# Optimization experiments

Hardware: AMD Instinct MI355X
Metric: run time of the kernel (lower is better)

The kernel has to match this reference:

```python
import jax, jax.numpy as jnp
import numpy as np


def setup_inputs() -> dict:
    key = jax.random.key(0)
    k1, k2, k3, k4 = jax.random.split(key, 4)
    batch, T, state_dim, action_dim = 64, 1024, 512, 128
    x0 = jax.random.normal(k1, (batch, state_dim), dtype=jnp.float32)
    us = jax.random.normal(k2, (batch, T, action_dim), dtype=jnp.float32)
    # Scale A so the 1024-step linear recurrence stays bounded (spectral radius < 1)
    A = jax.random.normal(k3, (state_dim, state_dim), dtype=jnp.float32) * (0.9 / np.sqrt(state_dim))
    B = jax.random.normal(k4, (action_dim, state_dim), dtype=jnp.float32) * (1.0 / np.sqrt(action_dim))
    return {"x0": x0, "us": us, "A": A, "B": B}


def reference(x0, us, A, B):
    """Linear SSM rollout: x_{t+1} = x_t @ A + u_t @ B, returns xs [batch, T, state_dim]."""
    us_t = jnp.swapaxes(us, 0, 1)  # [T, batch, action_dim]

    def step(x, u):
        x_next = x @ A + u @ B  # [batch, state_dim]
        return x_next, x_next

    _, xs = jax.lax.scan(step, x0, us_t)  # xs: [T, batch, state_dim]
    return jnp.swapaxes(xs, 0, 1)  # [batch, T, state_dim]
```

## Files before the change

### kernel.cpp

```cpp
#include <hip/hip_runtime.h>


typedef __attribute__((ext_vector_type(8))) short bf16x8;
typedef __attribute__((ext_vector_type(8))) unsigned short ushort8;
typedef __attribute__((ext_vector_type(4))) float f32x4;
typedef unsigned short ushort_t;

#define MFMA16(a, b, c) __builtin_amdgcn_mfma_f32_16x16x32_bf16(a, b, c, 0, 0, 0)

#define OFF_AT  0UL
#define OFF_AU  8912896UL
#define OFF_BT  15204352UL
#define OFF_BU  15335424UL
#define OFF_X0B 15466496UL
#define OFF_YPK 15532032UL
#define OFF_Z   23920640UL
#define OFF_ZS  49086464UL
#define OFF_E2  58523648UL

__host__ __device__ __forceinline__ int slot_of(int p) {
    if (p == 0) return 16;
    if (p <= 8) return p - 1;
    return 7 + (p >> 3);
}

__device__ __forceinline__ unsigned short f2bf(float f) {
    union { float f; unsigned u; } v; v.f = f;
    unsigned r = v.u + 0x7FFFu + ((v.u >> 16) & 1u);
    return (unsigned short)(r >> 16);
}

__device__ __forceinline__ float bf2f(ushort_t h) {
    union { unsigned u; float f; } v; v.u = ((unsigned)h) << 16; return v.f;
}

__device__ __forceinline__ int sel4(int4 v, int p) {
    return p == 0 ? v.x : p == 1 ? v.y : p == 2 ? v.z : v.w;
}

typedef __attribute__((address_space(3))) unsigned int as3_u32;
typedef __attribute__((address_space(1))) const unsigned int as1_u32;
__device__ __forceinline__ void gll16(const void* g, void* l) {
    __builtin_amdgcn_global_load_lds((as1_u32*)g, (as3_u32*)l, 16, 0, 0);
}

__global__ __launch_bounds__(256) void prep_kernel(const float* __restrict__ x0,
                                                   const float* __restrict__ us,
                                                   const float* __restrict__ A,
                                                   const float* __restrict__ B,
                                                   char* __restrict__ ws) {
    ushort_t* At1 = (ushort_t*)(ws + OFF_AT);
    ushort_t* Au1 = (ushort_t*)(ws + OFF_AU);
    ushort_t* Bt  = (ushort_t*)(ws + OFF_BT);
    ushort_t* Bu  = (ushort_t*)(ws + OFF_BU);
    ushort_t* X0b = (ushort_t*)(ws + OFF_X0B);
    ushort_t* Z   = (ushort_t*)(ws + OFF_Z);
    long idx = (long)blockIdx.x * 256 + threadIdx.x;
    if (idx < 262144) {
        int k = (int)(idx >> 9), n = (int)(idx & 511);
        ushort_t v = f2bf(A[idx]);
        Au1[idx] = v;
        At1[(long)n * 512 + k] = v;
    } else if (idx < 327680) {
        long i2 = idx - 262144;
        int kp = (int)(i2 >> 9), n = (int)(i2 & 511);
        ushort_t v = f2bf(B[i2]);
        Bt[(long)n * 128 + kp] = v;
        Bu[i2] = v;
    } else if (idx < 331776) {
        long gi = idx - 327680;
        long e0 = gi * 8;
        float4 v0 = *(const float4*)(x0 + e0);
        float4 v1 = *(const float4*)(x0 + e0 + 4);
        ushort8 h = { f2bf(v0.x), f2bf(v0.y), f2bf(v0.z), f2bf(v0.w),
                      f2bf(v1.x), f2bf(v1.y), f2bf(v1.z), f2bf(v1.w) };
        *(ushort8*)(X0b + e0) = h;
    } else if (idx < 1380352) {
        long gi = idx - 331776;
        int row = (int)(gi >> 7), g8 = (int)(gi & 127);
        int c = row >> 6, b = row & 63;
        const float* src = us + (long)b * 131072 + c * 1024 + g8 * 8;
        float4 v0 = *(const float4*)src;
        float4 v1 = *(const float4*)(src + 4);
        ushort8 h = { f2bf(v0.x), f2bf(v0.y), f2bf(v0.z), f2bf(v0.w),
                      f2bf(v1.x), f2bf(v1.y), f2bf(v1.z), f2bf(v1.w) };
        *(ushort8*)(Z + (long)row * 1536 + 512 + g8 * 8) = h;
    } else {
        long gi2 = idx - 1380352;
        if (gi2 < 262144) {
            int n = (int)(gi2 >> 9), k2 = (int)(gi2 & 511);
            At1[(long)16 * 262144 + gi2] = (n == k2) ? (ushort_t)0x3F80 : (ushort_t)0;
        }
    }
}

__global__ __launch_bounds__(256) void pow_stage(char* __restrict__ ws,
                                                 int4 dd, int4 mm, int4 ii, int dual) {
    __shared__ ushort_t ldsX[64 * 512];
    ushort_t* At = (ushort_t*)(ws + OFF_AT);
    ushort_t* Au = (ushort_t*)(ws + OFF_AU);

    int bx = blockIdx.x;
    int nb = bx & 3, mb = (bx >> 2) & 7;
    int prod, pair;
    if (dual) { prod = (bx >> 5) & 1; pair = bx >> 6; }
    else      { prod = 0;             pair = bx >> 5; }
    int d = sel4(dd, pair), m_ = sel4(mm, pair), i_ = sel4(ii, pair);

    const ushort_t *Xp, *Yp; ushort_t* outp;
    if (prod == 0) { Xp = At + (long)slot_of(m_) * 262144; Yp = Au + (long)slot_of(i_) * 262144; outp = At + (long)slot_of(d) * 262144; }
    else           { Xp = Au + (long)slot_of(i_) * 262144; Yp = At + (long)slot_of(m_) * 262144; outp = Au + (long)slot_of(d) * 262144; }

    int tid = threadIdx.x, w = tid >> 6, lane = tid & 63, q = lane >> 4, r = lane & 15;

    for (int i2 = tid; i2 < 64 * 64; i2 += 256) {
        int row = i2 >> 6, c8 = i2 & 63;
        ushort8 v = *(const ushort8*)(Xp + (long)(mb * 64 + row) * 512 + c8 * 8);
        *(ushort8*)&ldsX[row * 512 + ((c8 ^ (row & 7)) << 3)] = v;
    }
    __syncthreads();

    f32x4 acc[4][2];
    for (int a1 = 0; a1 < 4; a1++) for (int b1 = 0; b1 < 2; b1++) acc[a1][b1] = (f32x4){0.f, 0.f, 0.f, 0.f};

    int n0 = nb * 128 + w * 32;
    for (int kt = 0; kt < 16; kt++) {
        bf16x8 b0 = *(const bf16x8*)(Yp + (long)(n0 + r) * 512 + kt * 32 + q * 8);
        bf16x8 b1 = *(const bf16x8*)(Yp + (long)(n0 + 16 + r) * 512 + kt * 32 + q * 8);
        int g2 = kt * 4 + q;
#pragma unroll
        for (int mi = 0; mi < 4; mi++) {
            int row = mi * 16 + r;
            bf16x8 a = *(bf16x8*)&ldsX[row * 512 + ((g2 ^ (row & 7)) << 3)];
            acc[mi][0] = MFMA16(a, b0, acc[mi][0]);
            acc[mi][1] = MFMA16(a, b1, acc[mi][1]);
        }
    }
    for (int mi = 0; mi < 4; mi++) for (int nj = 0; nj < 2; nj++) {
        int m = mb * 64 + mi * 16 + q * 4, n = n0 + nj * 16 + r;
        for (int v = 0; v < 4; v++) outp[(long)(m + v) * 512 + n] = f2bf(acc[mi][nj][v]);
    }
}

__global__ __launch_bounds__(256) void wk_kernel(char* __restrict__ ws) {
    __shared__ ushort_t ldsX[64 * 512];
    ushort_t* At = (ushort_t*)(ws + OFF_AT);
    ushort_t* Bu = (ushort_t*)(ws + OFF_BU);
    ushort_t* Bt = (ushort_t*)(ws + OFF_BT);
    ushort_t* Ypk = (ushort_t*)(ws + OFF_YPK);

    int bx = blockIdx.x;
    int k8 = bx >> 3, mb = bx & 7;
    int tid = threadIdx.x, w = tid >> 6, lane = tid & 63, q = lane >> 4, r = lane & 15;

    if (k8 == 7) {
        for (int i2 = tid; i2 < 64 * 32; i2 += 256) {
            int row = i2 >> 5, c4 = i2 & 31;
            ushort4 v = *(const ushort4*)(Bt + (long)(mb * 64 + row) * 128 + c4 * 4);
            for (int k = 0; k < 8; k++)
                *(ushort4*)(Ypk + (long)k * 524288 + (long)(mb * 64 + row) * 1024 + k * 128 + c4 * 4) = v;
        }
        return;
    }

    int p = 7 - k8;
    const ushort_t* Xp = At + (long)slot_of(p) * 262144;
    for (int i2 = tid; i2 < 64 * 64; i2 += 256) {
        int row = i2 >> 6, c8 = i2 & 63;
        ushort8 v = *(const ushort8*)(Xp + (long)(mb * 64 + row) * 512 + c8 * 8);
        *(ushort8*)&ldsX[row * 512 + ((c8 ^ (row & 7)) << 3)] = v;
    }
    __syncthreads();

    f32x4 acc[4][2];
    for (int a1 = 0; a1 < 4; a1++) for (int b1 = 0; b1 < 2; b1++) acc[a1][b1] = (f32x4){0.f, 0.f, 0.f, 0.f};

    int n0 = w * 32;
    for (int kt = 0; kt < 16; kt++) {
        bf16x8 b0 = *(const bf16x8*)(Bu + (long)(n0 + r) * 512 + kt * 32 + q * 8);
        bf16x8 b1 = *(const bf16x8*)(Bu + (long)(n0 + 16 + r) * 512 + kt * 32 + q * 8);
        int g2 = kt * 4 + q;
#pragma unroll
        for (int mi = 0; mi < 4; mi++) {
            int row = mi * 16 + r;
            bf16x8 a = *(bf16x8*)&ldsX[row * 512 + ((g2 ^ (row & 7)) << 3)];
            acc[mi][0] = MFMA16(a, b0, acc[mi][0]);
            acc[mi][1] = MFMA16(a, b1, acc[mi][1]);
        }
    }
    for (int mi = 0; mi < 4; mi++) for (int nj = 0; nj < 2; nj++) {
        int m = mb * 64 + mi * 16 + q * 4, n = n0 + nj * 16 + r;
        for (int v = 0; v < 4; v++) {
            ushort_t h = f2bf(acc[mi][nj][v]);
            for (int k = p; k < 8; k++)
                Ypk[(long)k * 524288 + (long)(m + v) * 1024 + (k - p) * 128 + n] = h;
        }
    }
}

__global__ __launch_bounds__(256, 4) void e1g(char* __restrict__ ws) {
    __shared__ ushort_t Alds[64 * 64];
    __shared__ ushort_t Blds[128 * 64];
    const ushort_t* Z   = (const ushort_t*)(ws + OFF_Z);
    const ushort_t* Yw  = (const ushort_t*)(ws + OFF_YPK) + 7 * 524288;
    ushort_t* Zs = (ushort_t*)(ws + OFF_ZS);

    int bx = blockIdx.x;
    int c = bx >> 2, nt = bx & 3;
    int tid = threadIdx.x, w = tid >> 6, lane = tid & 63, q = lane >> 4, r = lane & 15;
    int wr = w >> 1, wc = w & 1;
    int l8 = lane >> 3, srcg = (lane & 7) ^ l8;

    f32x4 acc[2][4];
#pragma unroll
    for (int a1 = 0; a1 < 2; a1++)
#pragma unroll
        for (int b1 = 0; b1 < 4; b1++) acc[a1][b1] = (f32x4){0.f, 0.f, 0.f, 0.f};

    for (int s = 0; s < 16; s++) {
        int k0 = s * 64;
#pragma unroll
        for (int i = 0; i < 2; i++) {
            int row = i * 32 + w * 8 + l8;
            gll16(Z + (long)(c * 64 + row) * 1536 + 512 + k0 + srcg * 8,
                  &Alds[i * 2048 + w * 512]);
        }
#pragma unroll
        for (int i = 0; i < 4; i++) {
            int row = i * 32 + w * 8 + l8;
            gll16(Yw + (long)(nt * 128 + row) * 1024 + k0 + srcg * 8,
                  &Blds[i * 2048 + w * 512]);
        }
        __syncthreads();
#pragma unroll
        for (int kt = 0; kt < 2; kt++) {
            int g2 = kt * 4 + q;
            bf16x8 a[2], b[4];
#pragma unroll
            for (int mi = 0; mi < 2; mi++) {
                int row = wr * 32 + mi * 16 + r;
                a[mi] = *(bf16x8*)&Alds[row * 64 + ((g2 ^ (row & 7)) << 3)];
            }
#pragma unroll
            for (int nj = 0; nj < 4; nj++) {
                int row = wc * 64 + nj * 16 + r;
                b[nj] = *(bf16x8*)&Blds[row * 64 + ((g2 ^ (row & 7)) << 3)];
            }
#pragma unroll
            for (int mi = 0; mi < 2; mi++)
#pragma unroll
                for (int nj = 0; nj < 4; nj++)
                    acc[mi][nj] = MFMA16(a[mi], b[nj], acc[mi][nj]);
        }
        __syncthreads();
    }

    int g = c >> 3, cc = c & 7;
#pragma unroll
    for (int mi = 0; mi < 2; mi++)
#pragma unroll
        for (int nj = 0; nj < 4; nj++) {
            int brow = wr * 32 + mi * 16 + q * 4;
            int n = nt * 128 + wc * 64 + nj * 16 + r;
#pragma unroll
            for (int v = 0; v < 4; v++)
                Zs[(long)(g * 64 + brow + v) * 4608 + (1 + cc) * 512 + n] = f2bf(acc[mi][nj][v]);
        }
}

__global__ __launch_bounds__(256, 4) void e2g(char* __restrict__ ws) {
    __shared__ ushort_t Alds[64 * 64];
    __shared__ ushort_t Blds[64 * 64];
    const ushort_t* Zs = (const ushort_t*)(ws + OFF_ZS);
    const ushort_t* At = (const ushort_t*)(ws + OFF_AT);
    ushort_t* E2b = (ushort_t*)(ws + OFF_E2);

    int bx = blockIdx.x;
    int g = bx >> 3, ntb = bx & 7;
    int tid = threadIdx.x, w = tid >> 6, lane = tid & 63, q = lane >> 4, r = lane & 15;
    int wr = w >> 1, wc = w & 1;
    int l8 = lane >> 3, srcg = (lane & 7) ^ l8;

    f32x4 acc[2][2];
#pragma unroll
    for (int a1 = 0; a1 < 2; a1++)
#pragma unroll
        for (int b1 = 0; b1 < 2; b1++) acc[a1][b1] = (f32x4){0.f, 0.f, 0.f, 0.f};

    for (int s = 0; s < 8; s++) {
        const ushort_t* Yb = At + (long)slot_of(8 * (7 - s)) * 262144;
        for (int ks = 0; ks < 8; ks++) {
            int k0 = ks * 64;
#pragma unroll
            for (int i = 0; i < 2; i++) {
                int row = i * 32 + w * 8 + l8;
                gll16(Zs + (long)(g * 64 + row) * 4608 + (1 + s) * 512 + k0 + srcg * 8,
                      &Alds[i * 2048 + w * 512]);
                gll16(Yb + (long)(ntb * 64 + row) * 512 + k0 + srcg * 8,
                      &Blds[i * 2048 + w * 512]);
            }
            __syncthreads();
#pragma unroll
            for (int kt = 0; kt < 2; kt++) {
                int g2 = kt * 4 + q;
                bf16x8 a[2], b[2];
#pragma unroll
                for (int mi = 0; mi < 2; mi++) {
                    int row = wr * 32 + mi * 16 + r;
                    a[mi] = *(bf16x8*)&Alds[row * 64 + ((g2 ^ (row & 7)) << 3)];
                }
#pragma unroll
                for (int nj = 0; nj < 2; nj++) {
                    int row = wc * 32 + nj * 16 + r;
                    b[nj] = *(bf16x8*)&Blds[row * 64 + ((g2 ^ (row & 7)) << 3)];
                }
#pragma unroll
                for (int mi = 0; mi < 2; mi++)
#pragma unroll
                    for (int nj = 0; nj < 2; nj++)
                        acc[mi][nj] = MFMA16(a[mi], b[nj], acc[mi][nj]);
            }
            __syncthreads();
        }
    }

#pragma unroll
    for (int mi = 0; mi < 2; mi++)
#pragma unroll
        for (int nj = 0; nj < 2; nj++) {
            int brow = wr * 32 + mi * 16 + q * 4;
            int n = ntb * 64 + wc * 32 + nj * 16 + r;
#pragma unroll
            for (int v = 0; v < 4; v++)
                E2b[(long)g * 32768 + (long)(brow + v) * 512 + n] = f2bf(acc[mi][nj][v]);
        }
}

__global__ __launch_bounds__(256) void s2k(char* __restrict__ ws) {
    __shared__ ushort_t ldsX[64 * 512];
    ushort_t* At  = (ushort_t*)(ws + OFF_AT);
    ushort_t* E2b = (ushort_t*)(ws + OFF_E2);
    ushort_t* X0b = (ushort_t*)(ws + OFF_X0B);
    ushort_t* Zs  = (ushort_t*)(ws + OFF_ZS);

    int bx = blockIdx.x;
    int g = bx >> 2, nb = bx & 3;
    int tid = threadIdx.x, w = tid >> 6, lane = tid & 63, q = lane >> 4, r = lane & 15;

    int nterms = (g == 0) ? 1 : 2;

    f32x4 acc[4][2];
    for (int a1 = 0; a1 < 4; a1++) for (int b1 = 0; b1 < 2; b1++) acc[a1][b1] = (f32x4){0.f, 0.f, 0.f, 0.f};

    for (int t = 0; t < nterms; t++) {
        const ushort_t* X; const ushort_t* Y = nullptr;
        if (g == 0) { X = X0b; }
        else if (t == 0) { X = E2b + (long)(g - 1) * 32768; }
        else if (g == 1) { X = X0b; Y = At + (long)slot_of(64) * 262144; }
        else { X = E2b + (long)(g - 2) * 32768; Y = At + (long)slot_of(64) * 262144; }

        if (Y == nullptr) {
            int n0 = nb * 128 + w * 32;
            for (int mi = 0; mi < 4; mi++) for (int nj = 0; nj < 2; nj++) {
                int m = mi * 16 + q * 4, n = n0 + nj * 16 + r;
                for (int v = 0; v < 4; v++) acc[mi][nj][v] += bf2f(X[(long)(m + v) * 512 + n]);
            }
        } else {
            __syncthreads();
            for (int i2 = tid; i2 < 64 * 64; i2 += 256) {
                int row = i2 >> 6, c8 = i2 & 63;
                ushort8 v = *(const ushort8*)(X + (long)row * 512 + c8 * 8);
                *(ushort8*)&ldsX[row * 512 + ((c8 ^ (row & 7)) << 3)] = v;
            }
            __syncthreads();
            int n0 = nb * 128 + w * 32;
            for (int kt = 0; kt < 16; kt++) {
                bf16x8 b0 = *(const bf16x8*)(Y + (long)(n0 + r) * 512 + kt * 32 + q * 8);
                bf16x8 b1 = *(const bf16x8*)(Y + (long)(n0 + 16 + r) * 512 + kt * 32 + q * 8);
                int g2 = kt * 4 + q;
#pragma unroll
                for (int mi = 0; mi < 4; mi++) {
                    int row = mi * 16 + r;
                    bf16x8 a = *(bf16x8*)&ldsX[row * 512 + ((g2 ^ (row & 7)) << 3)];
                    acc[mi][0] = MFMA16(a, b0, acc[mi][0]);
                    acc[mi][1] = MFMA16(a, b1, acc[mi][1]);
                }
            }
        }
    }

    int n0 = nb * 128 + w * 32;
    for (int mi = 0; mi < 4; mi++) for (int nj = 0; nj < 2; nj++) {
        int m = mi * 16 + q * 4, n = n0 + nj * 16 + r;
        for (int v = 0; v < 4; v++)
            Zs[(long)(g * 64 + m + v) * 4608 + n] = f2bf(acc[mi][nj][v]);
    }
}

__global__ __launch_bounds__(256, 4) void s1g(char* __restrict__ ws) {
    __shared__ ushort_t Alds[64 * 64];
    __shared__ ushort_t Blds[128 * 64];
    const ushort_t* Zs = (const ushort_t*)(ws + OFF_ZS);
    const ushort_t* At = (const ushort_t*)(ws + OFF_AT);
    ushort_t* Z = (ushort_t*)(ws + OFF_Z);

    int bx = blockIdx.x;
    int j = bx & 7, nt = (bx >> 3) & 3, g = bx >> 5;
    int tid = threadIdx.x, w = tid >> 6, lane = tid & 63, q = lane >> 4, r = lane & 15;
    int wr = w >> 1, wc = w & 1;
    int l8 = lane >> 3, srcg = (lane & 7) ^ l8;

    f32x4 acc[2][4];
#pragma unroll
    for (int a1 = 0; a1 < 2; a1++)
#pragma unroll
        for (int b1 = 0; b1 < 4; b1++) acc[a1][b1] = (f32x4){0.f, 0.f, 0.f, 0.f};

    for (int s = 0; s <= j; s++) {
        int p = (s == 0) ? 8 * j : 8 * (j - s);
        const ushort_t* Yb = At + (long)slot_of(p) * 262144;
        for (int ks = 0; ks < 8; ks++) {
            int k0 = ks * 64;
#pragma unroll
            for (int i = 0; i < 2; i++) {
                int row = i * 32 + w * 8 + l8;
                gll16(Zs + (long)(g * 64 + row) * 4608 + s * 512 + k0 + srcg * 8,
                      &Alds[i * 2048 + w * 512]);
            }
#pragma unroll
            for (int i = 0; i < 4; i++) {
                int row = i * 32 + w * 8 + l8;
                gll16(Yb + (long)(nt * 128 + row) * 512 + k0 + srcg * 8,
                      &Blds[i * 2048 + w * 512]);
            }
            __syncthreads();
#pragma unroll
            for (int kt = 0; kt < 2; kt++) {
                int g2 = kt * 4 + q;
                bf16x8 a[2], b[4];
#pragma unroll
                for (int mi = 0; mi < 2; mi++) {
                    int row = wr * 32 + mi * 16 + r;
                    a[mi] = *(bf16x8*)&Alds[row * 64 + ((g2 ^ (row & 7)) << 3)];
                }
#pragma unroll
                for (int nj = 0; nj < 4; nj++) {
                    int row = wc * 64 + nj * 16 + r;
                    b[nj] = *(bf16x8*)&Blds[row * 64 + ((g2 ^ (row & 7)) << 3)];
                }
#pragma unroll
                for (int mi = 0; mi < 2; mi++)
#pragma unroll
                    for (int nj = 0; nj < 4; nj++)
                        acc[mi][nj] = MFMA16(a[mi], b[nj], acc[mi][nj]);
            }
            __syncthreads();
        }
    }

#pragma unroll
    for (int mi = 0; mi < 2; mi++)
#pragma unroll
        for (int nj = 0; nj < 4; nj++) {
            int brow = wr * 32 + mi * 16 + q * 4;
            int n = nt * 128 + wc * 64 + nj * 16 + r;
#pragma unroll
            for (int v = 0; v < 4; v++)
                Z[(long)(g * 512 + j * 64 + brow + v) * 1536 + n] = f2bf(acc[mi][nj][v]);
        }
}

__global__ __launch_bounds__(256, 4) void outg(float* __restrict__ dout,
                                               char* __restrict__ ws) {
    __shared__ ushort_t Alds[128 * 64];
    __shared__ ushort_t Blds[128 * 64];
    const ushort_t* Z   = (const ushort_t*)(ws + OFF_Z);
    const ushort_t* At  = (const ushort_t*)(ws + OFF_AT);
    const ushort_t* Ypk = (const ushort_t*)(ws + OFF_YPK);

    int bx = blockIdx.x;
    int mt = bx & 63;
    int k  = (bx >> 6) & 7;
    int nt = bx >> 9;
    int tid = threadIdx.x, w = tid >> 6, lane = tid & 63, q = lane >> 4, r = lane & 15;
    int wr = w >> 1, wc = w & 1;

    int Ks = 8 + 2 * (k + 1);
    const ushort_t* Ya = At + (long)slot_of(k + 1) * 262144;
    const ushort_t* Yu = Ypk + (long)k * 524288;

    int l8 = lane >> 3;
    int srcg = (lane & 7) ^ l8;

    f32x4 acc[4][4];
#pragma unroll
    for (int a1 = 0; a1 < 4; a1++)
#pragma unroll
        for (int b1 = 0; b1 < 4; b1++) acc[a1][b1] = (f32x4){0.f, 0.f, 0.f, 0.f};

    for (int s = 0; s < Ks; s++) {
        int k0 = s * 64;
#pragma unroll
        for (int i = 0; i < 4; i++) {
            int row = i * 32 + w * 8 + l8;
            gll16(Z + (long)(mt * 128 + row) * 1536 + k0 + srcg * 8,
                  &Alds[i * 2048 + w * 512]);
        }
        if (k0 < 512) {
#pragma unroll
            for (int i = 0; i < 4; i++) {
                int row = i * 32 + w * 8 + l8;
                gll16(Ya + (long)(nt * 128 + row) * 512 + k0 + srcg * 8,
                      &Blds[i * 2048 + w * 512]);
            }
        } else {
#pragma unroll
            for (int i = 0; i < 4; i++) {
                int row = i * 32 + w * 8 + l8;
                gll16(Yu + (long)(nt * 128 + row) * 1024 + (k0 - 512) + srcg * 8,
                      &Blds[i * 2048 + w * 512]);
            }
        }
        __syncthreads();
#pragma unroll
        for (int kt = 0; kt < 2; kt++) {
            int g2 = kt * 4 + q;
            bf16x8 a[4], b[4];
#pragma unroll
            for (int mi = 0; mi < 4; mi++) {
                int row = wr * 64 + mi * 16 + r;
                a[mi] = *(bf16x8*)&Alds[row * 64 + ((g2 ^ (row & 7)) << 3)];
            }
#pragma unroll
            for (int nj = 0; nj < 4; nj++) {
                int row = wc * 64 + nj * 16 + r;
                b[nj] = *(bf16x8*)&Blds[row * 64 + ((g2 ^ (row & 7)) << 3)];
            }
#pragma unroll
            for (int mi = 0; mi < 4; mi++)
#pragma unroll
                for (int nj = 0; nj < 4; nj++)
                    acc[mi][nj] = MFMA16(a[mi], b[nj], acc[mi][nj]);
        }
        __syncthreads();
    }

#pragma unroll
    for (int mi = 0; mi < 4; mi++) {
        int m = mt * 128 + wr * 64 + mi * 16 + q * 4;
#pragma unroll
        for (int nj = 0; nj < 4; nj++) {
            int n = nt * 128 + wc * 64 + nj * 16 + r;
#pragma unroll
            for (int v = 0; v < 4; v++) {
                int mm = m + v;
                dout[(long)(mm & 63) * 524288 + (long)(((mm >> 6) << 3) + k) * 512 + n] = acc[mi][nj][v];
            }
        }
    }
}

extern "C" void kernel_launch(void* const* d_in, const int* in_sizes, int n_in,
                              void* d_out, int out_size, void* d_ws, size_t ws_size,
                              hipStream_t stream) {
    const float* x0 = (const float*)d_in[0];
    const float* us = (const float*)d_in[1];
    const float* A  = (const float*)d_in[2];
    const float* B  = (const float*)d_in[3];
    float* dout = (float*)d_out;
    char* ws = (char*)d_ws;

    prep_kernel<<<6416, 256, 0, stream>>>(x0, us, A, B, ws);

    const int stn[6]     = {1, 2, 4, 1, 2, 4};
    const int stdual[6]  = {1, 1, 1, 1, 1, 0};
    const int std_[6][4] = {{2,0,0,0},{3,4,0,0},{5,6,7,8},{16,0,0,0},{24,32,0,0},{40,48,56,64}};
    const int stm[6][4]  = {{1,0,0,0},{2,2,0,0},{4,4,4,4},{8,0,0,0},{16,16,0,0},{32,32,32,32}};
    const int sti[6][4]  = {{1,0,0,0},{1,2,0,0},{1,2,3,4},{8,0,0,0},{8,16,0,0},{8,16,24,32}};
    for (int s = 0; s < 6; s++) {
        int4 dd = {std_[s][0], std_[s][1], std_[s][2], std_[s][3]};
        int4 mm = {stm[s][0], stm[s][1], stm[s][2], stm[s][3]};
        int4 ii = {sti[s][0], sti[s][1], sti[s][2], sti[s][3]};
        int blocks = stn[s] * (stdual[s] ? 64 : 32);
        pow_stage<<<blocks, 256, 0, stream>>>(ws, dd, mm, ii, stdual[s]);
    }

    wk_kernel<<<64, 256, 0, stream>>>(ws);
    e1g<<<512, 256, 0, stream>>>(ws);
    e2g<<<128, 256, 0, stream>>>(ws);
    s2k<<<64, 256, 0, stream>>>(ws);
    s1g<<<512, 256, 0, stream>>>(ws);
    outg<<<2048, 256, 0, stream>>>(dout, ws);
}
```

Baseline: 290.8 us.

## Restructure chunked scan stages with double-buffered LDS and direct global B loads

```diff
diff --git a/kernel.cpp b/kernel.cpp
--- a/kernel.cpp
+++ b/kernel.cpp
@@ -12,11 +12,10 @@
 #define OFF_AU  8912896UL
 #define OFF_BT  15204352UL
 #define OFF_BU  15335424UL
-#define OFF_X0B 15466496UL
-#define OFF_YPK 15532032UL
-#define OFF_Z   23920640UL
-#define OFF_ZS  49086464UL
-#define OFF_E2  58523648UL
+#define OFF_WT  15466496UL
+#define OFF_Z   16515072UL
+#define OFF_E1S 41680896UL
+#define OFF_E2S 50069504UL
 
 __host__ __device__ __forceinline__ int slot_of(int p) {
     if (p == 0) return 16;
@@ -28,10 +27,6 @@
     union { float f; unsigned u; } v; v.f = f;
     unsigned r = v.u + 0x7FFFu + ((v.u >> 16) & 1u);
     return (unsigned short)(r >> 16);
-}
-
-__device__ __forceinline__ float bf2f(ushort_t h) {
-    union { unsigned u; float f; } v; v.u = ((unsigned)h) << 16; return v.f;
 }
 
 __device__ __forceinline__ int sel4(int4 v, int p) {
@@ -53,7 +48,7 @@
     ushort_t* Au1 = (ushort_t*)(ws + OFF_AU);
     ushort_t* Bt  = (ushort_t*)(ws + OFF_BT);
     ushort_t* Bu  = (ushort_t*)(ws + OFF_BU);
-    ushort_t* X0b = (ushort_t*)(ws + OFF_X0B);
+    ushort_t* X0b = (ushort_t*)(ws + OFF_E2S);
     ushort_t* Z   = (ushort_t*)(ws + OFF_Z);
     long idx = (long)blockIdx.x * 256 + threadIdx.x;
     if (idx < 262144) {
@@ -147,7 +142,7 @@
     ushort_t* At = (ushort_t*)(ws + OFF_AT);
     ushort_t* Bu = (ushort_t*)(ws + OFF_BU);
     ushort_t* Bt = (ushort_t*)(ws + OFF_BT);
-    ushort_t* Ypk = (ushort_t*)(ws + OFF_YPK);
+    ushort_t* Wt = (ushort_t*)(ws + OFF_WT);
 
     int bx = blockIdx.x;
     int k8 = bx >> 3, mb = bx & 7;
@@ -157,8 +152,7 @@
         for (int i2 = tid; i2 < 64 * 32; i2 += 256) {
             int row = i2 >> 5, c4 = i2 & 31;
             ushort4 v = *(const ushort4*)(Bt + (long)(mb * 64 + row) * 128 + c4 * 4);
-            for (int k = 0; k < 8; k++)
-                *(ushort4*)(Ypk + (long)k * 524288 + (long)(mb * 64 + row) * 1024 + k * 128 + c4 * 4) = v;
+            *(ushort4*)(Wt + (long)(mb * 64 + row) * 128 + c4 * 4) = v;
         }
         return;
     }
@@ -188,22 +182,18 @@
             acc[mi][1] = MFMA16(a, b1, acc[mi][1]);
         }
     }
+    ushort_t* Wp = Wt + (long)p * 65536;
     for (int mi = 0; mi < 4; mi++) for (int nj = 0; nj < 2; nj++) {
         int m = mb * 64 + mi * 16 + q * 4, n = n0 + nj * 16 + r;
-        for (int v = 0; v < 4; v++) {
-            ushort_t h = f2bf(acc[mi][nj][v]);
-            for (int k = p; k < 8; k++)
-                Ypk[(long)k * 524288 + (long)(m + v) * 1024 + (k - p) * 128 + n] = h;
-        }
-    }
-}
-
-__global__ __launch_bounds__(256, 4) void e1g(char* __restrict__ ws) {
-    __shared__ ushort_t Alds[64 * 64];
-    __shared__ ushort_t Blds[128 * 64];
-    const ushort_t* Z   = (const ushort_t*)(ws + OFF_Z);
-    const ushort_t* Yw  = (const ushort_t*)(ws + OFF_YPK) + 7 * 524288;
-    ushort_t* Zs = (ushort_t*)(ws + OFF_ZS);
+        for (int v = 0; v < 4; v++) Wp[(long)(m + v) * 128 + n] = f2bf(acc[mi][nj][v]);
+    }
+}
+
+__global__ __launch_bounds__(256) void e1g(char* __restrict__ ws) {
+    __shared__ ushort_t Alds[2][64 * 64];
+    const ushort_t* Z  = (const ushort_t*)(ws + OFF_Z);
+    const ushort_t* Wt = (const ushort_t*)(ws + OFF_WT);
+    ushort_t* E1s = (ushort_t*)(ws + OFF_E1S);
 
     int bx = blockIdx.x;
     int c = bx >> 2, nt = bx & 3;
@@ -211,27 +201,33 @@
     int wr = w >> 1, wc = w & 1;
     int l8 = lane >> 3, srcg = (lane & 7) ^ l8;
 
+    const ushort_t* Xb = Z + (long)c * 64 * 1536 + 512;
+
     f32x4 acc[2][4];
 #pragma unroll
     for (int a1 = 0; a1 < 2; a1++)
 #pragma unroll
         for (int b1 = 0; b1 < 4; b1++) acc[a1][b1] = (f32x4){0.f, 0.f, 0.f, 0.f};
 
+#pragma unroll
+    for (int i = 0; i < 2; i++) {
+        int row = i * 32 + w * 8 + l8;
+        gll16(Xb + (long)row * 1536 + srcg * 8, &Alds[0][i * 2048 + w * 512]);
+    }
+    __syncthreads();
+
+    int cur = 0;
     for (int s = 0; s < 16; s++) {
-        int k0 = s * 64;
-#pragma unroll
-        for (int i = 0; i < 2; i++) {
-            int row = i * 32 + w * 8 + l8;
-            gll16(Z + (long)(c * 64 + row) * 1536 + 512 + k0 + srcg * 8,
-                  &Alds[i * 2048 + w * 512]);
-        }
-#pragma unroll
-        for (int i = 0; i < 4; i++) {
-            int row = i * 32 + w * 8 + l8;
-            gll16(Yw + (long)(nt * 128 + row) * 1024 + k0 + srcg * 8,
-                  &Blds[i * 2048 + w * 512]);
-        }
-        __syncthreads();
+        if (s + 1 < 16) {
+            int kn = (s + 1) * 64;
+#pragma unroll
+            for (int i = 0; i < 2; i++) {
+                int row = i * 32 + w * 8 + l8;
+                gll16(Xb + (long)row * 1536 + kn + srcg * 8, &Alds[cur ^ 1][i * 2048 + w * 512]);
+            }
+        }
+        const ushort_t* Yb = Wt + (long)(7 - (s >> 1)) * 65536;
+        int sub = (s & 1) * 64;
 #pragma unroll
         for (int kt = 0; kt < 2; kt++) {
             int g2 = kt * 4 + q;
@@ -239,12 +235,12 @@
 #pragma unroll
             for (int mi = 0; mi < 2; mi++) {
                 int row = wr * 32 + mi * 16 + r;
-                a[mi] = *(bf16x8*)&Alds[row * 64 + ((g2 ^ (row & 7)) << 3)];
+                a[mi] = *(bf16x8*)&Alds[cur][row * 64 + ((g2 ^ (row & 7)) << 3)];
             }
 #pragma unroll
             for (int nj = 0; nj < 4; nj++) {
-                int row = wc * 64 + nj * 16 + r;
-                b[nj] = *(bf16x8*)&Blds[row * 64 + ((g2 ^ (row & 7)) << 3)];
+                int n = nt * 128 + wc * 64 + nj * 16 + r;
+                b[nj] = *(const bf16x8*)(Yb + (long)n * 128 + sub + kt * 32 + q * 8);
             }
 #pragma unroll
             for (int mi = 0; mi < 2; mi++)
@@ -253,230 +249,194 @@
                     acc[mi][nj] = MFMA16(a[mi], b[nj], acc[mi][nj]);
         }
         __syncthreads();
-    }
-
-    int g = c >> 3, cc = c & 7;
+        cur ^= 1;
+    }
+
 #pragma unroll
     for (int mi = 0; mi < 2; mi++)
 #pragma unroll
         for (int nj = 0; nj < 4; nj++) {
-            int brow = wr * 32 + mi * 16 + q * 4;
+            int m = wr * 32 + mi * 16 + q * 4;
             int n = nt * 128 + wc * 64 + nj * 16 + r;
 #pragma unroll
             for (int v = 0; v < 4; v++)
-                Zs[(long)(g * 64 + brow + v) * 4608 + (1 + cc) * 512 + n] = f2bf(acc[mi][nj][v]);
-        }
-}
-
-__global__ __launch_bounds__(256, 4) void e2g(char* __restrict__ ws) {
-    __shared__ ushort_t Alds[64 * 64];
-    __shared__ ushort_t Blds[64 * 64];
-    const ushort_t* Zs = (const ushort_t*)(ws + OFF_ZS);
-    const ushort_t* At = (const ushort_t*)(ws + OFF_AT);
-    ushort_t* E2b = (ushort_t*)(ws + OFF_E2);
+                E1s[(long)c * 32768 + (long)(m + v) * 512 + n] = f2bf(acc[mi][nj][v]);
+        }
+}
+
+__global__ __launch_bounds__(256) void e2g(char* __restrict__ ws) {
+    __shared__ ushort_t Alds[2][64 * 64];
+    const ushort_t* At  = (const ushort_t*)(ws + OFF_AT);
+    const ushort_t* E1s = (const ushort_t*)(ws + OFF_E1S);
+    ushort_t* E2s = (ushort_t*)(ws + OFF_E2S);
 
     int bx = blockIdx.x;
-    int g = bx >> 3, ntb = bx & 7;
+    int g = bx >> 2, nt = bx & 3;
     int tid = threadIdx.x, w = tid >> 6, lane = tid & 63, q = lane >> 4, r = lane & 15;
     int wr = w >> 1, wc = w & 1;
     int l8 = lane >> 3, srcg = (lane & 7) ^ l8;
 
-    f32x4 acc[2][2];
+    f32x4 acc[2][4];
 #pragma unroll
     for (int a1 = 0; a1 < 2; a1++)
 #pragma unroll
-        for (int b1 = 0; b1 < 2; b1++) acc[a1][b1] = (f32x4){0.f, 0.f, 0.f, 0.f};
-
-    for (int s = 0; s < 8; s++) {
-        const ushort_t* Yb = At + (long)slot_of(8 * (7 - s)) * 262144;
-        for (int ks = 0; ks < 8; ks++) {
-            int k0 = ks * 64;
+        for (int b1 = 0; b1 < 4; b1++) acc[a1][b1] = (f32x4){0.f, 0.f, 0.f, 0.f};
+
+#pragma unroll
+    for (int i = 0; i < 2; i++) {
+        int row = i * 32 + w * 8 + l8;
+        gll16(E1s + (long)(8 * g) * 32768 + (long)row * 512 + srcg * 8,
+              &Alds[0][i * 2048 + w * 512]);
+    }
+    __syncthreads();
+
+    int cur = 0;
+    for (int s = 0; s < 64; s++) {
+        if (s + 1 < 64) {
+            int t2 = (s + 1) >> 3, kn = ((s + 1) & 7) * 64;
+            const ushort_t* Xp = E1s + (long)(8 * g + t2) * 32768;
 #pragma unroll
             for (int i = 0; i < 2; i++) {
                 int row = i * 32 + w * 8 + l8;
-                gll16(Zs + (long)(g * 64 + row) * 4608 + (1 + s) * 512 + k0 + srcg * 8,
-                      &Alds[i * 2048 + w * 512]);
-                gll16(Yb + (long)(ntb * 64 + row) * 512 + k0 + srcg * 8,
-                      &Blds[i * 2048 + w * 512]);
-            }
-            __syncthreads();
-#pragma unroll
-            for (int kt = 0; kt < 2; kt++) {
-                int g2 = kt * 4 + q;
-                bf16x8 a[2], b[2];
-#pragma unroll
-                for (int mi = 0; mi < 2; mi++) {
-                    int row = wr * 32 + mi * 16 + r;
-                    a[mi] = *(bf16x8*)&Alds[row * 64 + ((g2 ^ (row & 7)) << 3)];
-                }
-#pragma unroll
-                for (int nj = 0; nj < 2; nj++) {
-                    int row = wc * 32 + nj * 16 + r;
-                    b[nj] = *(bf16x8*)&Blds[row * 64 + ((g2 ^ (row & 7)) << 3)];
-                }
-#pragma unroll
-                for (int mi = 0; mi < 2; mi++)
-#pragma unroll
-                    for (int nj = 0; nj < 2; nj++)
-                        acc[mi][nj] = MFMA16(a[mi], b[nj], acc[mi][nj]);
-            }
-            __syncthreads();
-        }
+                gll16(Xp + (long)row * 512 + kn + srcg * 8, &Alds[cur ^ 1][i * 2048 + w * 512]);
+            }
+        }
+        int t = s >> 3, k0 = (s & 7) * 64;
+        const ushort_t* Yb = At + (long)slot_of(8 * (7 - t)) * 262144;
+#pragma unroll
+        for (int kt = 0; kt < 2; kt++) {
+            int g2 = kt * 4 + q;
+            bf16x8 a[2], b[4];
+#pragma unroll
+            for (int mi = 0; mi < 2; mi++) {
+                int row = wr * 32 + mi * 16 + r;
+                a[mi] = *(bf16x8*)&Alds[cur][row * 64 + ((g2 ^ (row & 7)) << 3)];
+            }
+#pragma unroll
+            for (int nj = 0; nj < 4; nj++) {
+                int n = nt * 128 + wc * 64 + nj * 16 + r;
+                b[nj] = *(const bf16x8*)(Yb + (long)n * 512 + k0 + kt * 32 + q * 8);
+            }
+#pragma unroll
+            for (int mi = 0; mi < 2; mi++)
+#pragma unroll
+                for (int nj = 0; nj < 4; nj++)
+                    acc[mi][nj] = MFMA16(a[mi], b[nj], acc[mi][nj]);
+        }
+        __syncthreads();
+        cur ^= 1;
     }
 
 #pragma unroll
     for (int mi = 0; mi < 2; mi++)
 #pragma unroll
-        for (int nj = 0; nj < 2; nj++) {
-            int brow = wr * 32 + mi * 16 + q * 4;
-            int n = ntb * 64 + wc * 32 + nj * 16 + r;
+        for (int nj = 0; nj < 4; nj++) {
+            int m = wr * 32 + mi * 16 + q * 4;
+            int n = nt * 128 + wc * 64 + nj * 16 + r;
 #pragma unroll
             for (int v = 0; v < 4; v++)
-                E2b[(long)g * 32768 + (long)(brow + v) * 512 + n] = f2bf(acc[mi][nj][v]);
-        }
-}
-
-__global__ __launch_bounds__(256) void s2k(char* __restrict__ ws) {
-    __shared__ ushort_t ldsX[64 * 512];
-    ushort_t* At  = (ushort_t*)(ws + OFF_AT);
-    ushort_t* E2b = (ushort_t*)(ws + OFF_E2);
-    ushort_t* X0b = (ushort_t*)(ws + OFF_X0B);
-    ushort_t* Zs  = (ushort_t*)(ws + OFF_ZS);
+                E2s[(long)(1 + g) * 32768 + (long)(m + v) * 512 + n] = f2bf(acc[mi][nj][v]);
+        }
+}
+
+__global__ __launch_bounds__(256) void s1x(char* __restrict__ ws) {
+    __shared__ ushort_t Alds[2][64 * 64];
+    const ushort_t* At  = (const ushort_t*)(ws + OFF_AT);
+    const ushort_t* E1s = (const ushort_t*)(ws + OFF_E1S);
+    const ushort_t* E2s = (const ushort_t*)(ws + OFF_E2S);
+    ushort_t* Z = (ushort_t*)(ws + OFF_Z);
 
     int bx = blockIdx.x;
-    int g = bx >> 2, nb = bx & 3;
-    int tid = threadIdx.x, w = tid >> 6, lane = tid & 63, q = lane >> 4, r = lane & 15;
-
-    int nterms = (g == 0) ? 1 : 2;
-
-    f32x4 acc[4][2];
-    for (int a1 = 0; a1 < 4; a1++) for (int b1 = 0; b1 < 2; b1++) acc[a1][b1] = (f32x4){0.f, 0.f, 0.f, 0.f};
-
-    for (int t = 0; t < nterms; t++) {
-        const ushort_t* X; const ushort_t* Y = nullptr;
-        if (g == 0) { X = X0b; }
-        else if (t == 0) { X = E2b + (long)(g - 1) * 32768; }
-        else if (g == 1) { X = X0b; Y = At + (long)slot_of(64) * 262144; }
-        else { X = E2b + (long)(g - 2) * 32768; Y = At + (long)slot_of(64) * 262144; }
-
-        if (Y == nullptr) {
-            int n0 = nb * 128 + w * 32;
-            for (int mi = 0; mi < 4; mi++) for (int nj = 0; nj < 2; nj++) {
-                int m = mi * 16 + q * 4, n = n0 + nj * 16 + r;
-                for (int v = 0; v < 4; v++) acc[mi][nj][v] += bf2f(X[(long)(m + v) * 512 + n]);
-            }
-        } else {
-            __syncthreads();
-            for (int i2 = tid; i2 < 64 * 64; i2 += 256) {
-                int row = i2 >> 6, c8 = i2 & 63;
-                ushort8 v = *(const ushort8*)(X + (long)row * 512 + c8 * 8);
-                *(ushort8*)&ldsX[row * 512 + ((c8 ^ (row & 7)) << 3)] = v;
-            }
-            __syncthreads();
-            int n0 = nb * 128 + w * 32;
-            for (int kt = 0; kt < 16; kt++) {
-                bf16x8 b0 = *(const bf16x8*)(Y + (long)(n0 + r) * 512 + kt * 32 + q * 8);
-                bf16x8 b1 = *(const bf16x8*)(Y + (long)(n0 + 16 + r) * 512 + kt * 32 + q * 8);
-                int g2 = kt * 4 + q;
-#pragma unroll
-                for (int mi = 0; mi < 4; mi++) {
-                    int row = mi * 16 + r;
-                    bf16x8 a = *(bf16x8*)&ldsX[row * 512 + ((g2 ^ (row & 7)) << 3)];
-                    acc[mi][0] = MFMA16(a, b0, acc[mi][0]);
-                    acc[mi][1] = MFMA16(a, b1, acc[mi][1]);
-                }
-            }
-        }
-    }
-
-    int n0 = nb * 128 + w * 32;
-    for (int mi = 0; mi < 4; mi++) for (int nj = 0; nj < 2; nj++) {
-        int m = mi * 16 + q * 4, n = n0 + nj * 16 + r;
-        for (int v = 0; v < 4; v++)
-            Zs[(long)(g * 64 + m + v) * 4608 + n] = f2bf(acc[mi][nj][v]);
-    }
-}
-
-__global__ __launch_bounds__(256, 4) void s1g(char* __restrict__ ws) {
-    __shared__ ushort_t Alds[64 * 64];
-    __shared__ ushort_t Blds[128 * 64];
-    const ushort_t* Zs = (const ushort_t*)(ws + OFF_ZS);
-    const ushort_t* At = (const ushort_t*)(ws + OFF_AT);
-    ushort_t* Z = (ushort_t*)(ws + OFF_Z);
-
-    int bx = blockIdx.x;
-    int j = bx & 7, nt = (bx >> 3) & 3, g = bx >> 5;
+    int c = bx >> 2, nt = bx & 3;
+    int g = c >> 3, j = c & 7;
+    int extra = (j == 0 && g >= 1) ? 1 : 0;
+    int nterms = 1 + extra + j;
+    int S = nterms * 8;
     int tid = threadIdx.x, w = tid >> 6, lane = tid & 63, q = lane >> 4, r = lane & 15;
     int wr = w >> 1, wc = w & 1;
     int l8 = lane >> 3, srcg = (lane & 7) ^ l8;
 
+    auto xptr = [&](int t) -> const ushort_t* {
+        if (t == 0) return E2s + (long)g * 32768;
+        if (extra && t == 1) return E2s + (long)(g - 1) * 32768;
+        return E1s + (long)(8 * g + t - 1 - extra) * 32768;
+    };
+    auto yptr = [&](int t) -> const ushort_t* {
+        int p = (t == 0) ? 8 * j : ((extra && t == 1) ? 64 : 8 * (j - t + extra));
+        return At + (long)slot_of(p) * 262144;
+    };
+
     f32x4 acc[2][4];
 #pragma unroll
     for (int a1 = 0; a1 < 2; a1++)
 #pragma unroll
         for (int b1 = 0; b1 < 4; b1++) acc[a1][b1] = (f32x4){0.f, 0.f, 0.f, 0.f};
 
-    for (int s = 0; s <= j; s++) {
-        int p = (s == 0) ? 8 * j : 8 * (j - s);
-        const ushort_t* Yb = At + (long)slot_of(p) * 262144;
-        for (int ks = 0; ks < 8; ks++) {
-            int k0 = ks * 64;
+    {
+        const ushort_t* Xp = xptr(0);
+#pragma unroll
+        for (int i = 0; i < 2; i++) {
+            int row = i * 32 + w * 8 + l8;
+            gll16(Xp + (long)row * 512 + srcg * 8, &Alds[0][i * 2048 + w * 512]);
+        }
+    }
+    __syncthreads();
+
+    int cur = 0;
+    for (int s = 0; s < S; s++) {
+        if (s + 1 < S) {
+            const ushort_t* Xp = xptr((s + 1) >> 3);
+            int kn = ((s + 1) & 7) * 64;
 #pragma unroll
             for (int i = 0; i < 2; i++) {
                 int row = i * 32 + w * 8 + l8;
-                gll16(Zs + (long)(g * 64 + row) * 4608 + s * 512 + k0 + srcg * 8,
-                      &Alds[i * 2048 + w * 512]);
-            }
-#pragma unroll
-            for (int i = 0; i < 4; i++) {
-                int row = i * 32 + w * 8 + l8;
-                gll16(Yb + (long)(nt * 128 + row) * 512 + k0 + srcg * 8,
-                      &Blds[i * 2048 + w * 512]);
-            }
-            __syncthreads();
-#pragma unroll
-            for (int kt = 0; kt < 2; kt++) {
-                int g2 = kt * 4 + q;
-                bf16x8 a[2], b[4];
-#pragma unroll
-                for (int mi = 0; mi < 2; mi++) {
-                    int row = wr * 32 + mi * 16 + r;
-                    a[mi] = *(bf16x8*)&Alds[row * 64 + ((g2 ^ (row & 7)) << 3)];
-                }
-#pragma unroll
-                for (int nj = 0; nj < 4; nj++) {
-                    int row = wc * 64 + nj * 16 + r;
-                    b[nj] = *(bf16x8*)&Blds[row * 64 + ((g2 ^ (row & 7)) << 3)];
-                }
-#pragma unroll
-                for (int mi = 0; mi < 2; mi++)
-#pragma unroll
-                    for (int nj = 0; nj < 4; nj++)
-                        acc[mi][nj] = MFMA16(a[mi], b[nj], acc[mi][nj]);
-            }
-            __syncthreads();
-        }
+                gll16(Xp + (long)row * 512 + kn + srcg * 8, &Alds[cur ^ 1][i * 2048 + w * 512]);
+            }
+        }
+        int k0 = (s & 7) * 64;
+        const ushort_t* Yb = yptr(s >> 3);
+#pragma unroll
+        for (int kt = 0; kt < 2; kt++) {
+            int g2 = kt * 4 + q;
+            bf16x8 a[2], b[4];
+#pragma unroll
+            for (int mi = 0; mi < 2; mi++) {
+                int row = wr * 32 + mi * 16 + r;
+                a[mi] = *(bf16x8*)&Alds[cur][row * 64 + ((g2 ^ (row & 7)) << 3)];
+            }
+#pragma unroll
+            for (int nj = 0; nj < 4; nj++) {
+                int n = nt * 128 + wc * 64 + nj * 16 + r;
+                b[nj] = *(const bf16x8*)(Yb + (long)n * 512 + k0 + kt * 32 + q * 8);
+            }
+#pragma unroll
+            for (int mi = 0; mi < 2; mi++)
+#pragma unroll
+                for (int nj = 0; nj < 4; nj++)
+                    acc[mi][nj] = MFMA16(a[mi], b[nj], acc[mi][nj]);
+        }
+        __syncthreads();
+        cur ^= 1;
     }
 
 #pragma unroll
     for (int mi = 0; mi < 2; mi++)
 #pragma unroll
         for (int nj = 0; nj < 4; nj++) {
-            int brow = wr * 32 + mi * 16 + q * 4;
+            int m = wr * 32 + mi * 16 + q * 4;
             int n = nt * 128 + wc * 64 + nj * 16 + r;
 #pragma unroll
             for (int v = 0; v < 4; v++)
-                Z[(long)(g * 512 + j * 64 + brow + v) * 1536 + n] = f2bf(acc[mi][nj][v]);
-        }
-}
-
-__global__ __launch_bounds__(256, 4) void outg(float* __restrict__ dout,
-                                               char* __restrict__ ws) {
-    __shared__ ushort_t Alds[128 * 64];
-    __shared__ ushort_t Blds[128 * 64];
-    const ushort_t* Z   = (const ushort_t*)(ws + OFF_Z);
-    const ushort_t* At  = (const ushort_t*)(ws + OFF_AT);
-    const ushort_t* Ypk = (const ushort_t*)(ws + OFF_YPK);
+                Z[(long)(c * 64 + m + v) * 1536 + n] = f2bf(acc[mi][nj][v]);
+        }
+}
+
+__global__ __launch_bounds__(256) void outg(float* __restrict__ dout,
+                                            char* __restrict__ ws) {
+    __shared__ ushort_t Alds[2][128 * 64];
+    const ushort_t* Z  = (const ushort_t*)(ws + OFF_Z);
+    const ushort_t* At = (const ushort_t*)(ws + OFF_AT);
+    const ushort_t* Wt = (const ushort_t*)(ws + OFF_WT);
 
     int bx = blockIdx.x;
     int mt = bx & 63;
@@ -484,13 +444,11 @@
     int nt = bx >> 9;
     int tid = threadIdx.x, w = tid >> 6, lane = tid & 63, q = lane >> 4, r = lane & 15;
     int wr = w >> 1, wc = w & 1;
-
+    int l8 = lane >> 3, srcg = (lane & 7) ^ l8;
+
+    const ushort_t* Xb = Z + (long)mt * 128 * 1536;
+    const ushort_t* Ya = At + (long)slot_of(k + 1) * 262144;
     int Ks = 8 + 2 * (k + 1);
-    const ushort_t* Ya = At + (long)slot_of(k + 1) * 262144;
-    const ushort_t* Yu = Ypk + (long)k * 524288;
-
-    int l8 = lane >> 3;
-    int srcg = (lane & 7) ^ l8;
 
     f32x4 acc[4][4];
 #pragma unroll
@@ -498,30 +456,27 @@
 #pragma unroll
         for (int b1 = 0; b1 < 4; b1++) acc[a1][b1] = (f32x4){0.f, 0.f, 0.f, 0.f};
 
+#pragma unroll
+    for (int i = 0; i < 4; i++) {
+        int row = i * 32 + w * 8 + l8;
+        gll16(Xb + (long)row * 1536 + srcg * 8, &Alds[0][i * 2048 + w * 512]);
+    }
+    __syncthreads();
+
+    int cur = 0;
     for (int s = 0; s < Ks; s++) {
-        int k0 = s * 64;
-#pragma unroll
-        for (int i = 0; i < 4; i++) {
-            int row = i * 32 + w * 8 + l8;
-            gll16(Z + (long)(mt * 128 + row) * 1536 + k0 + srcg * 8,
-                  &Alds[i * 2048 + w * 512]);
-        }
-        if (k0 < 512) {
+        if (s + 1 < Ks) {
+            int kn = (s + 1) * 64;
 #pragma unroll
             for (int i = 0; i < 4; i++) {
                 int row = i * 32 + w * 8 + l8;
-                gll16(Ya + (long)(nt * 128 + row) * 512 + k0 + srcg * 8,
-                      &Blds[i * 2048 + w * 512]);
-            }
-        } else {
-#pragma unroll
-            for (int i = 0; i < 4; i++) {
-                int row = i * 32 + w * 8 + l8;
-                gll16(Yu + (long)(nt * 128 + row) * 1024 + (k0 - 512) + srcg * 8,
-                      &Blds[i * 2048 + w * 512]);
-            }
-        }
-        __syncthreads();
+                gll16(Xb + (long)row * 1536 + kn + srcg * 8, &Alds[cur ^ 1][i * 2048 + w * 512]);
+            }
+        }
+        int k0 = s * 64;
+        const ushort_t* Yb; int pitch, col;
+        if (k0 < 512) { Yb = Ya; pitch = 512; col = k0; }
+        else { int uc = k0 - 512; Yb = Wt + (long)(k - (uc >> 7)) * 65536; pitch = 128; col = uc & 127; }
 #pragma unroll
         for (int kt = 0; kt < 2; kt++) {
             int g2 = kt * 4 + q;
@@ -529,12 +484,12 @@
 #pragma unroll
             for (int mi = 0; mi < 4; mi++) {
                 int row = wr * 64 + mi * 16 + r;
-                a[mi] = *(bf16x8*)&Alds[row * 64 + ((g2 ^ (row & 7)) << 3)];
+                a[mi] = *(bf16x8*)&Alds[cur][row * 64 + ((g2 ^ (row & 7)) << 3)];
             }
 #pragma unroll
             for (int nj = 0; nj < 4; nj++) {
-                int row = wc * 64 + nj * 16 + r;
-                b[nj] = *(bf16x8*)&Blds[row * 64 + ((g2 ^ (row & 7)) << 3)];
+                int n = nt * 128 + wc * 64 + nj * 16 + r;
+                b[nj] = *(const bf16x8*)(Yb + (long)n * pitch + col + kt * 32 + q * 8);
             }
 #pragma unroll
             for (int mi = 0; mi < 4; mi++)
@@ -543,6 +498,7 @@
                     acc[mi][nj] = MFMA16(a[mi], b[nj], acc[mi][nj]);
         }
         __syncthreads();
+        cur ^= 1;
     }
 
 #pragma unroll
@@ -587,8 +543,7 @@
 
     wk_kernel<<<64, 256, 0, stream>>>(ws);
     e1g<<<512, 256, 0, stream>>>(ws);
-    e2g<<<128, 256, 0, stream>>>(ws);
-    s2k<<<64, 256, 0, stream>>>(ws);
-    s1g<<<512, 256, 0, stream>>>(ws);
+    e2g<<<64, 256, 0, stream>>>(ws);
+    s1x<<<512, 256, 0, stream>>>(ws);
     outg<<<2048, 256, 0, stream>>>(dout, ws);
 }
```

Result: slower. 488.1 us (+67.9%).
